# Performance work log

Hardware: AMD Instinct MI355X
Metric: run time of the kernel (lower is better)

The kernel has to match this reference:

```python
import jax, jax.numpy as jnp
import numpy as np
from functools import partial

GRAD_THR = 0.01
COUNT_THR = 3
MIN_PROB = 0.1
MAX_PROB = 0.9
FREE_PROB = 1e-10
HEIGHT_Q = 0.7


def prob2logodds(p):
    return jnp.log(p) - jnp.log1p(-p)


def shift_diff(x, d):
    # right neighbor minus left neighbor at dilation d (replicate padding on width)
    xp = jnp.pad(x, [(0, 0)] * (x.ndim - 1) + [(d, d)], mode='edge')
    return xp[..., 2 * d:] - xp[..., :-2 * d]


def assign_score(depth):
    rml_dx = jax.nn.relu(shift_diff(depth, 1))    # relu(right - left)
    lmr_dx = jax.nn.relu(-shift_diff(depth, 1))   # relu(left - right)
    rml_ddx = jax.nn.relu(-shift_diff(rml_dx, 2))  # relu(-(right-left))
    lmr_ddx = jax.nn.relu(shift_diff(lmr_dx, 2))   # relu(-(left-right))
    W = depth.shape[-1]
    grad_pos = jnp.concatenate([rml_ddx[..., :W // 2], lmr_ddx[..., W // 2:]], axis=-1)
    grad_neg = jnp.concatenate([lmr_ddx[..., :W // 2], rml_ddx[..., W // 2:]], axis=-1)
    return grad_pos, grad_neg


def _occupancy_one(xyz, score, g_mask, size, grad_thr, count_thr):
    # xyz: [3, N]; score, g_mask: [N]
    x, y, z = xyz[0], xyz[1], xyz[2]
    range_mask = (x >= 0) & (x <= size - 1) & (z >= 0) & (z <= size - 1)
    height_mask = y < jnp.quantile(y, HEIGHT_Q)
    valid = height_mask & range_mask
    obj = valid & (~g_mask) & (score > 0)
    ground = valid & g_mask
    xi = jnp.clip(x.astype(jnp.int32), 0, size - 1)
    zi = jnp.clip(z.astype(jnp.int32), 0, size - 1)
    idx = xi + size * zi  # [N] flat grid index
    G = size * size
    occ = jnp.zeros(G, jnp.float32).at[idx].add(
        jnp.where(obj & (score > grad_thr), 1.0, 0.0))
    norm = jnp.zeros(G, jnp.float32).at[idx].add(obj.astype(jnp.float32))
    gcnt = jnp.zeros(G, jnp.float32).at[idx].add(ground.astype(jnp.float32))
    free = (gcnt > 0) & (norm == 0)
    unknown = (~free) & (norm < count_thr)
    prob = occ / jnp.maximum(norm, 1.0)
    prob = jnp.where(unknown | free, 0.5, prob)
    return prob, free, unknown


def compute_occupancy_probability(scaled_ptcloud, ground_flat, disc_flat, size, grad_thr, count_thr):
    f = partial(_occupancy_one, size=size, grad_thr=grad_thr, count_thr=count_thr)
    return jax.vmap(f)(scaled_ptcloud, disc_flat, ground_flat)


def max_pool3x3(x):
    return jax.lax.reduce_window(
        x, -jnp.inf, jax.lax.max,
        (1, 1, 3, 3), (1, 1, 1, 1),
        [(0, 0), (0, 0), (1, 1), (1, 1)])


def setup_inputs() -> dict:
    key = jax.random.key(0)
    k1, k2, k3 = jax.random.split(key, 3)
    B, H, W, S = 32, 384, 1280, 256
    N = H * W
    depth = jax.random.uniform(k1, (B, 1, H, W), jnp.float32, 0.1, 80.0)
    ptc = jax.random.uniform(k2, (B, 3, N), jnp.float32, -5.0, float(S) + 5.0)
    gmask = jax.random.randint(k3, (B, 1, H, W), 0, 2).astype(bool)
    return {"depth": depth, "scaled_ptcloud": ptc, "ground_mask": gmask, "ogm_size": S}


def reference(depth, scaled_ptcloud, ground_mask, ogm_size):
    B = depth.shape[0]
    S = ogm_size
    prior_free_odds = prob2logodds(FREE_PROB)
    p_min_odds = prob2logodds(MIN_PROB)
    p_max_odds = prob2logodds(MAX_PROB)
    n_max_odds = prob2logodds(MAX_PROB)

    grad_pos, grad_neg = assign_score(depth)
    gp_flat = grad_pos.reshape(B, -1)
    gn_flat = grad_neg.reshape(B, -1)
    gm_flat = ground_mask.reshape(B, -1)

    pos_prob, free, unknown = compute_occupancy_probability(
        scaled_ptcloud, gm_flat, gp_flat, S, GRAD_THR, COUNT_THR)
    pos_odds = prob2logodds(pos_prob)
    pos_odds = jnp.where(free, prior_free_odds, pos_odds)
    pos_odds = jnp.where(unknown, 0.0, pos_odds)
    pos_odds = jnp.clip(pos_odds, p_min_odds, p_max_odds)

    neg_prob, _, _ = compute_occupancy_probability(
        scaled_ptcloud, gm_flat, gn_flat, S, GRAD_THR, COUNT_THR)
    neg_odds = prob2logodds(neg_prob)
    neg_odds = jnp.where(free | unknown, 0.0, neg_odds)
    neg_odds = jnp.clip(neg_odds, 0.0, n_max_odds)
    neg_odds = max_pool3x3(neg_odds.reshape(B, 1, S, S))

    return pos_odds.reshape(B, 1, S, S) - neg_odds
```

## Files before the change

kernel.cpp:

```cpp
#include <hip/hip_runtime.h>
#include <stdint.h>

#define H_    384
#define W_    1280
#define NPTS  (H_ * W_)
#define S_    256
#define G_    (S_ * S_)
#define NBH   32
#define NBC   32
#define NBS   480
#define NBF   64
#define NBINS 4096
#define QCAP  1024
#define LO_   (-16.0f)
#define INVW_ (4096.0f / 544.0f)
#define PMAX  2.1972246f
#define TX 64
#define TZ 16

typedef unsigned int u32;
typedef unsigned long long u64;
typedef unsigned char u8;
typedef float f32x4 __attribute__((ext_vector_type(4)));
typedef u32   u32x4 __attribute__((ext_vector_type(4)));

__device__ __forceinline__ u32 fkey(float f) {
    u32 u = __float_as_uint(f);
    return (u & 0x80000000u) ? ~u : (u | 0x80000000u);
}
__device__ __forceinline__ float keyfloat(u32 k) {
    u32 u = (k & 0x80000000u) ? (k ^ 0x80000000u) : ~k;
    return __uint_as_float(u);
}
__device__ __forceinline__ int lbin(float y) {
    int b = (int)floorf((y - LO_) * INVW_);
    return b < 0 ? 0 : (b > NBINS - 1 ? NBINS - 1 : b);
}
template<int NBB>
__device__ __forceinline__ void decode(int id, int& b, int& j) {
    const int r = id & 7;
    const int g8 = id >> 3;
    j = g8 % NBB;
    b = (g8 / NBB) * 8 + r;
}

__global__ void k_hist(const float* __restrict__ ptc, const u8* __restrict__ gmb,
                       u32* __restrict__ hgsum, u32* __restrict__ mode,
                       u32* __restrict__ pk, u8* __restrict__ gflag) {
    __shared__ u32 h[NBINS];
    int b, j; decode<NBH>((int)blockIdx.x, b, j);
    const int t = threadIdx.x;
    if (b == 0 && j == 0 && t < 64) {
        u32 v = ((const u32*)gmb)[t];
        bool bad = !(v == 0u || v == 1u || v == 0x3F800000u);
        u64 m = __ballot(bad);
        if (t == 0) *mode = (m == 0ULL) ? 1u : 0u;
    }
    {
        const u32x4 z4 = {0u, 0u, 0u, 0u};
        u32x4* pk4 = (u32x4*)(pk + (size_t)b * G_) + (size_t)j * (G_ / 4 / NBH);
        for (int k = t; k < G_ / 4 / NBH; k += 256) pk4[k] = z4;
        u32x4* gf4 = (u32x4*)(gflag + (size_t)b * G_) + (size_t)j * (G_ / 16 / NBH);
        if (t < G_ / 16 / NBH) gf4[t] = z4;
    }
    for (int k = t; k < NBINS; k += 256) h[k] = 0u;
    __syncthreads();
    const f32x4* y4 = (const f32x4*)(ptc + (size_t)b * 3 * NPTS + NPTS);
    for (int i = j * 256 + t; i < NPTS / 4; i += NBH * 256) {
        f32x4 v = y4[i];
        atomicAdd(&h[lbin(v.x)], 1u);
        atomicAdd(&h[lbin(v.y)], 1u);
        atomicAdd(&h[lbin(v.z)], 1u);
        atomicAdd(&h[lbin(v.w)], 1u);
    }
    __syncthreads();
    u32* dst = hgsum + (size_t)b * NBINS;
    for (int k = t; k < NBINS; k += 256)
        if (h[k]) atomicAdd(&dst[k], h[k]);
}

__global__ void k_find(const u32* __restrict__ hgsum, u32* __restrict__ fbuf, int ka) {
    __shared__ u32 h[NBINS];
    __shared__ u32 part[256];
    __shared__ u32 sres[4];
    const int t = threadIdx.x, b = blockIdx.x;
    const u32* src = hgsum + (size_t)b * NBINS;
    for (int k = t; k < NBINS; k += 256) h[k] = src[k];
    __syncthreads();
    u32 loc = 0;
#pragma unroll
    for (int q = 0; q < NBINS / 256; q++) loc += h[t * (NBINS / 256) + q];
    part[t] = loc;
    __syncthreads();
    for (int ofs = 1; ofs < 256; ofs <<= 1) {
        u32 v = (t >= ofs) ? part[t - ofs] : 0u;
        __syncthreads();
        part[t] += v;
        __syncthreads();
    }
    u32 before = part[t] - loc;
    const u32 ra = (u32)ka, rb = (u32)ka + 1u;
#pragma unroll
    for (int q = 0; q < NBINS / 256; q++) {
        const int jj = t * (NBINS / 256) + q;
        const u32 v = h[jj];
        if (before <= ra && ra < before + v) { sres[0] = (u32)jj; sres[1] = ra - before; }
        if (before <= rb && rb < before + v) { sres[2] = (u32)jj; sres[3] = rb - before; }
        before += v;
    }
    __syncthreads();
    if (t < 4) fbuf[b * 4 + t] = sres[t];
}

__global__ void k_collect(const float* __restrict__ ptc, const u32* __restrict__ fbuf,
                          u32* __restrict__ cnt, u32* __restrict__ cbuf) {
    int b, j; decode<NBC>((int)blockIdx.x, b, j);
    const int t = threadIdx.x;
    const int binA = (int)fbuf[b * 4 + 0];
    const int binB = (int)fbuf[b * 4 + 2];
    const bool twob = (binB != binA);
    const f32x4* y4 = (const f32x4*)(ptc + (size_t)b * 3 * NPTS + NPTS);
    u32* bufA = cbuf + (size_t)b * 2 * QCAP;
    u32* bufB = bufA + QCAP;
    for (int i = j * 256 + t; i < NPTS / 4; i += NBC * 256) {
        f32x4 v = y4[i];
        float f[4] = {v.x, v.y, v.z, v.w};
#pragma unroll
        for (int q = 0; q < 4; q++) {
            const int bn = lbin(f[q]);
            if (bn == binA) {
                u32 p = atomicAdd(&cnt[b * 2], 1u);
                if (p < QCAP) bufA[p] = fkey(f[q]);
            } else if (twob && bn == binB) {
                u32 p = atomicAdd(&cnt[b * 2 + 1], 1u);
                if (p < QCAP) bufB[p] = fkey(f[q]);
            }
        }
    }
}

__global__ void k_select(const u32* __restrict__ fbuf, const u32* __restrict__ cnt,
                         const u32* __restrict__ cbuf, float* __restrict__ tbuf,
                         float wlo, float whi) {
    __shared__ u32 sA[QCAP];
    __shared__ u32 sB[QCAP];
    __shared__ u32 skey[2];
    const int t = threadIdx.x, b = blockIdx.x;
    const u32 remA = fbuf[b * 4 + 1], remB = fbuf[b * 4 + 3];
    const bool twob = (fbuf[b * 4 + 0] != fbuf[b * 4 + 2]);
    u32 cA = cnt[b * 2];     if (cA > QCAP) cA = QCAP;
    u32 cB = cnt[b * 2 + 1]; if (cB > QCAP) cB = QCAP;
    const u32* bufA = cbuf + (size_t)b * 2 * QCAP;
    const u32* bufB = bufA + QCAP;
    for (u32 i = t; i < cA; i += 256) sA[i] = bufA[i];
    if (twob) for (u32 i = t; i < cB; i += 256) sB[i] = bufB[i];
    __syncthreads();
    for (u32 i = t; i < cA; i += 256) {
        const u32 k = sA[i];
        u32 less = 0, eq = 0;
        for (u32 jj = 0; jj < cA; jj++) { u32 kj = sA[jj]; less += (kj < k); eq += (kj == k); }
        if (less <= remA && remA < less + eq) skey[0] = k;
    }
    const u32* srcb = twob ? sB : sA;
    const u32 mB = twob ? cB : cA;
    for (u32 i = t; i < mB; i += 256) {
        const u32 k = srcb[i];
        u32 less = 0, eq = 0;
        for (u32 jj = 0; jj < mB; jj++) { u32 kj = srcb[jj]; less += (kj < k); eq += (kj == k); }
        if (less <= remB && remB < less + eq) skey[1] = k;
    }
    __syncthreads();
    if (t == 0) {
        float ylo = keyfloat(skey[0]);
        float yhi = keyfloat(skey[1]);
        tbuf[b] = __fadd_rn(__fmul_rn(ylo, wlo), __fmul_rn(yhi, whi));
    }
}

__global__ void k_scatter(const float* __restrict__ depth, const float* __restrict__ ptc,
                          const u8* __restrict__ gmb, const float* __restrict__ tbuf,
                          const u32* __restrict__ mode,
                          u32* __restrict__ pk, u8* __restrict__ gflag) {
    int b, j; decode<NBS>((int)blockIdx.x, b, j);
    const int t = threadIdx.x;
    const float st = tbuf[b];
    const u32 smode = *mode;
    const int i4 = j * 256 + t;
    const int i0 = i4 * 4;
    const size_t pb = (size_t)b * 3 * NPTS;

    const f32x4 yv = __builtin_nontemporal_load((const f32x4*)(ptc + pb + NPTS) + i4);
    const float fy[4] = {yv.x, yv.y, yv.z, yv.w};
    bool pass[4]; bool any = false;
#pragma unroll
    for (int q = 0; q < 4; q++) { pass[q] = fy[q] < st; any = any || pass[q]; }
    if (!any) return;

    const f32x4 xv = __builtin_nontemporal_load((const f32x4*)(ptc + pb) + i4);
    const f32x4 zv = __builtin_nontemporal_load((const f32x4*)(ptc + pb + 2 * NPTS) + i4);
    const float fx[4] = {xv.x, xv.y, xv.z, xv.w};
    const float fz[4] = {zv.x, zv.y, zv.z, zv.w};
    u32 gw[4];
    if (smode) {
        u32x4 gg = __builtin_nontemporal_load((const u32x4*)((const u32*)gmb + (size_t)b * NPTS) + i4);
        gw[0] = gg.x; gw[1] = gg.y; gw[2] = gg.z; gw[3] = gg.w;
    } else {
        u32 gg = __builtin_nontemporal_load((const u32*)(gmb + (size_t)b * NPTS) + i4);
        gw[0] = gg & 0xFFu; gw[1] = (gg >> 8) & 0xFFu; gw[2] = (gg >> 16) & 0xFFu; gw[3] = (gg >> 24) & 0xFFu;
    }

    const int colbase = i0 % W_;
    const float* drow = depth + (size_t)b * NPTS + (i0 - colbase);
    u32* pkb = pk + (size_t)b * G_;
    u8* gfb = gflag + (size_t)b * G_;

#pragma unroll
    for (int q = 0; q < 4; q++) {
        if (!pass[q]) continue;
        const float x = fx[q], z = fz[q];
        if (!(x >= 0.0f && x <= 255.0f && z >= 0.0f && z <= 255.0f)) continue;
        const int cell = (int)x + S_ * (int)z;
        if (gw[q]) { gfb[cell] = 1; continue; }

        const int col = colbase + q;
        int j1 = col - 2; if (j1 < 0) j1 = 0;
        int j2 = col + 2; if (j2 > W_ - 1) j2 = W_ - 1;
        int am = j1 - 1;  if (am < 0) am = 0;
        int ap = j1 + 1;  if (ap > W_ - 1) ap = W_ - 1;
        int bm = j2 - 1;  if (bm < 0) bm = 0;
        int bp = j2 + 1;  if (bp > W_ - 1) bp = W_ - 1;
        float a = drow[ap] - drow[am];
        float c = drow[bp] - drow[bm];
        float rml1 = fmaxf(a, 0.0f),  lmr1 = fmaxf(-a, 0.0f);
        float rml2 = fmaxf(c, 0.0f),  lmr2 = fmaxf(-c, 0.0f);
        float rddx = fmaxf(rml1 - rml2, 0.0f);
        float lddx = fmaxf(lmr2 - lmr1, 0.0f);
        float sp, sn;
        if (col < W_ / 2) { sp = rddx; sn = lddx; } else { sp = lddx; sn = rddx; }
        u32 p = (sp > 0.0f) ? (1u | ((u32)(sp > 0.01f) << 8)) : 0u;
        u32 n = (sn > 0.0f) ? ((1u << 16) | ((u32)(sn > 0.01f) << 24)) : 0u;
        const u32 inc = p | n;
        if (inc) atomicAdd(&pkb[cell], inc);
    }
}

__device__ __forceinline__ float neg_val(u32 w) {
    const u32 pn = w & 0xFFu;
    if (pn < 3u) return 0.0f;
    const u32 nn = (w >> 16) & 0xFFu;
    if (nn < 3u) return 0.0f;
    const u32 no = (w >> 24) & 0xFFu;
    float p = (float)no / (float)nn;
    float v = logf(p) - log1pf(-p);
    return fminf(fmaxf(v, 0.0f), PMAX);
}

__global__ void k_finalpool(const u32* __restrict__ pk, const u8* __restrict__ gflag,
                            float* __restrict__ out) {
    __shared__ float ng[(TZ + 2) * (TX + 2)];
    int b, j; decode<NBF>((int)blockIdx.x, b, j);
    const int t = threadIdx.x;
    const int x0 = (j & 3) * TX;
    const int z0 = (j >> 2) * TZ;
    const u32* pkb = pk + (size_t)b * G_;
    const u8* gfb = gflag + (size_t)b * G_;
    for (int idx = t; idx < (TZ + 2) * (TX + 2); idx += 256) {
        const int gx = x0 + idx % (TX + 2) - 1;
        const int gz = z0 + idx / (TX + 2) - 1;
        float v = -INFINITY;
        if (gx >= 0 && gx < S_ && gz >= 0 && gz < S_) v = neg_val(pkb[gx + S_ * gz]);
        ng[idx] = v;
    }
    __syncthreads();
    const int lx = t & 63;
    const int lz0 = (t >> 6) * 4;
#pragma unroll
    for (int k = 0; k < 4; k++) {
        const int lz = lz0 + k;
        const int cell = (x0 + lx) + S_ * (z0 + lz);
        const u32 w = pkb[cell];
        const u32 pn = w & 0xFFu;
        float po;
        if (pn < 3u) {
            po = (pn == 0u && gfb[cell]) ? -PMAX : 0.0f;
        } else {
            const u32 oc = (w >> 8) & 0xFFu;
            float p = (float)oc / (float)pn;
            float v = logf(p) - log1pf(-p);
            po = fminf(fmaxf(v, -PMAX), PMAX);
        }
        float mx = -INFINITY;
#pragma unroll
        for (int dz = 0; dz < 3; dz++)
#pragma unroll
            for (int dx = 0; dx < 3; dx++)
                mx = fmaxf(mx, ng[(lz + dz) * (TX + 2) + (lx + dx)]);
        out[(size_t)b * G_ + cell] = po - mx;
    }
}

extern "C" void kernel_launch(void* const* d_in, const int* in_sizes, int n_in,
                              void* d_out, int out_size, void* d_ws, size_t ws_size,
                              hipStream_t stream) {
    const float* depth = (const float*)d_in[0];
    const float* ptc   = (const float*)d_in[1];
    const u8* gm       = (const u8*)d_in[2];
    const int B = in_sizes[0] / NPTS;

    char* ws = (char*)d_ws;
    size_t off = 0;
    auto alloc = [&](size_t bytes) -> void* {
        void* p = ws + off; off += (bytes + 255) & ~(size_t)255; return p;
    };
    u32* hgsum = (u32*)alloc((size_t)B * NBINS * 4);
    u32* cnt   = (u32*)alloc((size_t)B * 2 * 4);
    const size_t zero_bytes = off;
    u32* pk    = (u32*)alloc((size_t)B * G_ * 4);
    u8*  gflag = (u8*)alloc((size_t)B * G_);
    u32* cbuf  = (u32*)alloc((size_t)B * 2 * QCAP * 4);
    float* tbuf= (float*)alloc((size_t)B * 4);
    u32* fbuf  = (u32*)alloc((size_t)B * 4 * 4);
    u32* mode  = (u32*)alloc(4);
    (void)ws_size; (void)n_in; (void)out_size;

    (void)hipMemsetAsync(d_ws, 0, zero_bytes, stream);

    const float idxf = 0.7f * (float)(NPTS - 1);
    const int   ka   = (int)floorf(idxf);
    const float whi  = idxf - (float)ka;
    const float wlo  = 1.0f - whi;

    k_hist    <<<dim3(NBH * B), dim3(256), 0, stream>>>(ptc, gm, hgsum, mode, pk, gflag);
    k_find    <<<dim3(B),       dim3(256), 0, stream>>>(hgsum, fbuf, ka);
    k_collect <<<dim3(NBC * B), dim3(256), 0, stream>>>(ptc, fbuf, cnt, cbuf);
    k_select  <<<dim3(B),       dim3(256), 0, stream>>>(fbuf, cnt, cbuf, tbuf, wlo, whi);
    k_scatter <<<dim3(NBS * B), dim3(256), 0, stream>>>(depth, ptc, gm, tbuf, mode, pk, gflag);
    k_finalpool<<<dim3(NBF * B), dim3(256), 0, stream>>>(pk, gflag, (float*)d_out);
}
```

Measured before the change: 512.5 us.

## Precompute per-pixel score and ground codes in histogram kernel for scatter

Moves the depth-gradient score and ground-mask evaluation out of the scatter kernel into the histogram kernel, which now reads depth with vector loads and writes a one-byte code per pixel. The scatter kernel then reads only one u32 per four points instead of scattered depth samples and the ground mask. The aim is to take the dependent gather loads off the scatter kernel's critical path and overlap that work with the histogram pass. In exchange the prep kernel always reads all of depth and the mask and writes an extra B*NPTS byte buffer, including for points that later fail the height test. Mode detection moves to a per-block shared flag.

Result: slower. 531.3 us (+3.7%).

```diff
diff --git a/kernel.cpp b/kernel.cpp
--- a/kernel.cpp
+++ b/kernel.cpp
@@ -7,6 +7,8 @@
 #define S_    256
 #define G_    (S_ * S_)
 #define NBH   32
+#define NSEG  (NPTS / NBH)
+#define NGRP  (NSEG / 4)
 #define NBC   32
 #define NBS   480
 #define NBF   64
@@ -44,18 +46,30 @@
     b = (g8 / NBB) * 8 + r;
 }
 
-__global__ void k_hist(const float* __restrict__ ptc, const u8* __restrict__ gmb,
-                       u32* __restrict__ hgsum, u32* __restrict__ mode,
-                       u32* __restrict__ pk, u8* __restrict__ gflag) {
+__device__ __forceinline__ u32 score_bits(float a, float cc, int col, u32 g) {
+    const float rml1 = fmaxf(a, 0.0f),  lmr1 = fmaxf(-a, 0.0f);
+    const float rml2 = fmaxf(cc, 0.0f), lmr2 = fmaxf(-cc, 0.0f);
+    const float rddx = fmaxf(rml1 - rml2, 0.0f);
+    const float lddx = fmaxf(lmr2 - lmr1, 0.0f);
+    float sp, sn;
+    if (col < W_ / 2) { sp = rddx; sn = lddx; } else { sp = lddx; sn = rddx; }
+    u32 c = 0;
+    c |= (sp > 0.0f)  ? 1u : 0u;
+    c |= (sp > 0.01f) ? 2u : 0u;
+    c |= (sn > 0.0f)  ? 4u : 0u;
+    c |= (sn > 0.01f) ? 8u : 0u;
+    c |= g ? 16u : 0u;
+    return c;
+}
+
+__global__ void k_prep(const float* __restrict__ depth, const float* __restrict__ ptc,
+                       const u8* __restrict__ gmb, u32* __restrict__ hgsum,
+                       u8* __restrict__ scode, u32* __restrict__ pk,
+                       u8* __restrict__ gflag) {
     __shared__ u32 h[NBINS];
+    __shared__ u32 smode;
     int b, j; decode<NBH>((int)blockIdx.x, b, j);
     const int t = threadIdx.x;
-    if (b == 0 && j == 0 && t < 64) {
-        u32 v = ((const u32*)gmb)[t];
-        bool bad = !(v == 0u || v == 1u || v == 0x3F800000u);
-        u64 m = __ballot(bad);
-        if (t == 0) *mode = (m == 0ULL) ? 1u : 0u;
-    }
     {
         const u32x4 z4 = {0u, 0u, 0u, 0u};
         u32x4* pk4 = (u32x4*)(pk + (size_t)b * G_) + (size_t)j * (G_ / 4 / NBH);
@@ -64,7 +78,65 @@
         if (t < G_ / 16 / NBH) gf4[t] = z4;
     }
     for (int k = t; k < NBINS; k += 256) h[k] = 0u;
-    __syncthreads();
+    if (t < 64) {
+        u32 v = ((const u32*)gmb)[t];
+        bool bad = !(v == 0u || v == 1u || v == 0x3F800000u);
+        u64 m = __ballot(bad);
+        if (t == 0) smode = (m == 0ULL) ? 1u : 0u;
+    }
+    __syncthreads();
+    const u32 md = smode;
+
+    const int seg0 = j * NSEG;
+    const float* dbat = depth + (size_t)b * NPTS;
+    const u32* gmw = (const u32*)gmb;
+    u32* sc4 = (u32*)(scode + (size_t)b * NPTS + seg0);
+    for (int gi = t; gi < NGRP; gi += 256) {
+        const int i0 = seg0 + gi * 4;
+        const int c0 = i0 % W_;
+        const float* dr = dbat + (i0 - c0);
+        float aa[4], cca[4];
+        if (c0 >= 4 && c0 <= W_ - 8) {
+            const f32x4 v0 = *(const f32x4*)(dr + c0 - 4);
+            const f32x4 v1 = *(const f32x4*)(dr + c0);
+            const f32x4 v2 = *(const f32x4*)(dr + c0 + 4);
+            const float w[12] = {v0.x, v0.y, v0.z, v0.w, v1.x, v1.y, v1.z, v1.w,
+                                 v2.x, v2.y, v2.z, v2.w};
+#pragma unroll
+            for (int q = 0; q < 4; q++) {
+                aa[q]  = w[q + 3] - w[q + 1];
+                cca[q] = w[q + 7] - w[q + 5];
+            }
+        } else {
+#pragma unroll
+            for (int q = 0; q < 4; q++) {
+                const int c = c0 + q;
+                int j1 = c - 2; if (j1 < 0) j1 = 0;
+                int j2 = c + 2; if (j2 > W_ - 1) j2 = W_ - 1;
+                int am = j1 - 1; if (am < 0) am = 0;
+                int ap = j1 + 1; if (ap > W_ - 1) ap = W_ - 1;
+                int bm = j2 - 1; if (bm < 0) bm = 0;
+                int bp = j2 + 1; if (bp > W_ - 1) bp = W_ - 1;
+                aa[q]  = dr[ap] - dr[am];
+                cca[q] = dr[bp] - dr[bm];
+            }
+        }
+        u32 gw[4];
+        if (md) {
+            const u32x4 gg = *(const u32x4*)(gmw + (size_t)b * NPTS + i0);
+            gw[0] = gg.x; gw[1] = gg.y; gw[2] = gg.z; gw[3] = gg.w;
+        } else {
+            const u32 gg = *(const u32*)(gmb + (size_t)b * NPTS + i0);
+            gw[0] = gg & 0xFFu; gw[1] = (gg >> 8) & 0xFFu;
+            gw[2] = (gg >> 16) & 0xFFu; gw[3] = (gg >> 24) & 0xFFu;
+        }
+        u32 code = 0;
+#pragma unroll
+        for (int q = 0; q < 4; q++)
+            code |= score_bits(aa[q], cca[q], c0 + q, gw[q]) << (8 * q);
+        __builtin_nontemporal_store(code, sc4 + gi);
+    }
+
     const f32x4* y4 = (const f32x4*)(ptc + (size_t)b * 3 * NPTS + NPTS);
     for (int i = j * 256 + t; i < NPTS / 4; i += NBH * 256) {
         f32x4 v = y4[i];
@@ -177,16 +249,13 @@
     }
 }
 
-__global__ void k_scatter(const float* __restrict__ depth, const float* __restrict__ ptc,
-                          const u8* __restrict__ gmb, const float* __restrict__ tbuf,
-                          const u32* __restrict__ mode,
+__global__ void k_scatter(const float* __restrict__ ptc, const float* __restrict__ tbuf,
+                          const u8* __restrict__ scode,
                           u32* __restrict__ pk, u8* __restrict__ gflag) {
     int b, j; decode<NBS>((int)blockIdx.x, b, j);
     const int t = threadIdx.x;
     const float st = tbuf[b];
-    const u32 smode = *mode;
     const int i4 = j * 256 + t;
-    const int i0 = i4 * 4;
     const size_t pb = (size_t)b * 3 * NPTS;
 
     const f32x4 yv = __builtin_nontemporal_load((const f32x4*)(ptc + pb + NPTS) + i4);
@@ -198,19 +267,10 @@
 
     const f32x4 xv = __builtin_nontemporal_load((const f32x4*)(ptc + pb) + i4);
     const f32x4 zv = __builtin_nontemporal_load((const f32x4*)(ptc + pb + 2 * NPTS) + i4);
+    const u32 code4 = __builtin_nontemporal_load((const u32*)(scode + (size_t)b * NPTS) + i4);
     const float fx[4] = {xv.x, xv.y, xv.z, xv.w};
     const float fz[4] = {zv.x, zv.y, zv.z, zv.w};
-    u32 gw[4];
-    if (smode) {
-        u32x4 gg = __builtin_nontemporal_load((const u32x4*)((const u32*)gmb + (size_t)b * NPTS) + i4);
-        gw[0] = gg.x; gw[1] = gg.y; gw[2] = gg.z; gw[3] = gg.w;
-    } else {
-        u32 gg = __builtin_nontemporal_load((const u32*)(gmb + (size_t)b * NPTS) + i4);
-        gw[0] = gg & 0xFFu; gw[1] = (gg >> 8) & 0xFFu; gw[2] = (gg >> 16) & 0xFFu; gw[3] = (gg >> 24) & 0xFFu;
-    }
-
-    const int colbase = i0 % W_;
-    const float* drow = depth + (size_t)b * NPTS + (i0 - colbase);
+
     u32* pkb = pk + (size_t)b * G_;
     u8* gfb = gflag + (size_t)b * G_;
 
@@ -220,25 +280,10 @@
         const float x = fx[q], z = fz[q];
         if (!(x >= 0.0f && x <= 255.0f && z >= 0.0f && z <= 255.0f)) continue;
         const int cell = (int)x + S_ * (int)z;
-        if (gw[q]) { gfb[cell] = 1; continue; }
-
-        const int col = colbase + q;
-        int j1 = col - 2; if (j1 < 0) j1 = 0;
-        int j2 = col + 2; if (j2 > W_ - 1) j2 = W_ - 1;
-        int am = j1 - 1;  if (am < 0) am = 0;
-        int ap = j1 + 1;  if (ap > W_ - 1) ap = W_ - 1;
-        int bm = j2 - 1;  if (bm < 0) bm = 0;
-        int bp = j2 + 1;  if (bp > W_ - 1) bp = W_ - 1;
-        float a = drow[ap] - drow[am];
-        float c = drow[bp] - drow[bm];
-        float rml1 = fmaxf(a, 0.0f),  lmr1 = fmaxf(-a, 0.0f);
-        float rml2 = fmaxf(c, 0.0f),  lmr2 = fmaxf(-c, 0.0f);
-        float rddx = fmaxf(rml1 - rml2, 0.0f);
-        float lddx = fmaxf(lmr2 - lmr1, 0.0f);
-        float sp, sn;
-        if (col < W_ / 2) { sp = rddx; sn = lddx; } else { sp = lddx; sn = rddx; }
-        u32 p = (sp > 0.0f) ? (1u | ((u32)(sp > 0.01f) << 8)) : 0u;
-        u32 n = (sn > 0.0f) ? ((1u << 16) | ((u32)(sn > 0.01f) << 24)) : 0u;
+        const u32 cq = (code4 >> (8 * q)) & 0xFFu;
+        if (cq & 16u) { gfb[cell] = 1; continue; }
+        u32 p = (cq & 1u) ? (1u | (((cq >> 1) & 1u) << 8)) : 0u;
+        u32 n = (cq & 4u) ? ((1u << 16) | (((cq >> 3) & 1u) << 24)) : 0u;
         const u32 inc = p | n;
         if (inc) atomicAdd(&pkb[cell], inc);
     }
@@ -320,7 +365,7 @@
     u32* cbuf  = (u32*)alloc((size_t)B * 2 * QCAP * 4);
     float* tbuf= (float*)alloc((size_t)B * 4);
     u32* fbuf  = (u32*)alloc((size_t)B * 4 * 4);
-    u32* mode  = (u32*)alloc(4);
+    u8* scode  = (u8*)alloc((size_t)B * NPTS);
     (void)ws_size; (void)n_in; (void)out_size;
 
     (void)hipMemsetAsync(d_ws, 0, zero_bytes, stream);
@@ -330,10 +375,10 @@
     const float whi  = idxf - (float)ka;
     const float wlo  = 1.0f - whi;
 
-    k_hist    <<<dim3(NBH * B), dim3(256), 0, stream>>>(ptc, gm, hgsum, mode, pk, gflag);
+    k_prep    <<<dim3(NBH * B), dim3(256), 0, stream>>>(depth, ptc, gm, hgsum, scode, pk, gflag);
     k_find    <<<dim3(B),       dim3(256), 0, stream>>>(hgsum, fbuf, ka);
     k_collect <<<dim3(NBC * B), dim3(256), 0, stream>>>(ptc, fbuf, cnt, cbuf);
     k_select  <<<dim3(B),       dim3(256), 0, stream>>>(fbuf, cnt, cbuf, tbuf, wlo, whi);
-    k_scatter <<<dim3(NBS * B), dim3(256), 0, stream>>>(depth, ptc, gm, tbuf, mode, pk, gflag);
+    k_scatter <<<dim3(NBS * B), dim3(256), 0, stream>>>(ptc, tbuf, scode, pk, gflag);
     k_finalpool<<<dim3(NBF * B), dim3(256), 0, stream>>>(pk, gflag, (float*)d_out);
 }
```

## Fuse bin-find and select into collect kernel, pack ground flag into counts

Applied to the files above, without the earlier changes.

Each collect block now recomputes the quantile bin search from the global histogram with a wave-shuffle scan. The last block per batch, detected through an atomic done counter, performs the exact selection, which removes the separate find and select launches. The ground flag byte array is replaced by the top bit of the packed count word, set with atomicOr, so the flag zeroing and the extra reads in the final kernel go away. The costs are a redundant bin search in every collect block, a last-block-done pattern that depends on correct memory fences, and atomics on the ground path.

New measurement: 690.7 us. 1.35x slower.

```diff
diff --git a/kernel.cpp b/kernel.cpp
--- a/kernel.cpp
+++ b/kernel.cpp
@@ -24,6 +24,7 @@
 typedef float f32x4 __attribute__((ext_vector_type(4)));
 typedef u32   u32x4 __attribute__((ext_vector_type(4)));
 
+
 __device__ __forceinline__ u32 fkey(float f) {
     u32 u = __float_as_uint(f);
     return (u & 0x80000000u) ? ~u : (u | 0x80000000u);
@@ -44,9 +45,9 @@
     b = (g8 / NBB) * 8 + r;
 }
 
-__global__ void k_hist(const float* __restrict__ ptc, const u8* __restrict__ gmb,
+__global__ void k_prep(const float* __restrict__ ptc, const u8* __restrict__ gmb,
                        u32* __restrict__ hgsum, u32* __restrict__ mode,
-                       u32* __restrict__ pk, u8* __restrict__ gflag) {
+                       u32* __restrict__ pk) {
     __shared__ u32 h[NBINS];
     int b, j; decode<NBH>((int)blockIdx.x, b, j);
     const int t = threadIdx.x;
@@ -60,8 +61,6 @@
         const u32x4 z4 = {0u, 0u, 0u, 0u};
         u32x4* pk4 = (u32x4*)(pk + (size_t)b * G_) + (size_t)j * (G_ / 4 / NBH);
         for (int k = t; k < G_ / 4 / NBH; k += 256) pk4[k] = z4;
-        u32x4* gf4 = (u32x4*)(gflag + (size_t)b * G_) + (size_t)j * (G_ / 16 / NBH);
-        if (t < G_ / 16 / NBH) gf4[t] = z4;
     }
     for (int k = t; k < NBINS; k += 256) h[k] = 0u;
     __syncthreads();
@@ -79,46 +78,54 @@
         if (h[k]) atomicAdd(&dst[k], h[k]);
 }
 
-__global__ void k_find(const u32* __restrict__ hgsum, u32* __restrict__ fbuf, int ka) {
-    __shared__ u32 h[NBINS];
-    __shared__ u32 part[256];
+__device__ __forceinline__ void find_bins(const u32* __restrict__ hgsum, int b, int ka,
+                                          u32* sres, u32* swsum) {
+    const int t = threadIdx.x, lane = t & 63, w = t >> 6;
+    const u32x4* src = (const u32x4*)(hgsum + (size_t)b * NBINS) + t * 4;
+    const u32x4 a0 = src[0], a1 = src[1], a2 = src[2], a3 = src[3];
+    u32 v[16] = {a0.x, a0.y, a0.z, a0.w, a1.x, a1.y, a1.z, a1.w,
+                 a2.x, a2.y, a2.z, a2.w, a3.x, a3.y, a3.z, a3.w};
+    u32 loc = 0;
+#pragma unroll
+    for (int q = 0; q < 16; q++) loc += v[q];
+    u32 inc = loc;
+#pragma unroll
+    for (int off = 1; off < 64; off <<= 1) {
+        u32 n = __shfl_up(inc, off);
+        if (lane >= off) inc += n;
+    }
+    if (lane == 63) swsum[w] = inc;
+    __syncthreads();
+    u32 before = inc - loc;
+    for (int k = 0; k < w; k++) before += swsum[k];
+    const u32 ra = (u32)ka, rb = (u32)ka + 1u;
+#pragma unroll
+    for (int q = 0; q < 16; q++) {
+        const u32 c = v[q];
+        if (before <= ra && ra < before + c) { sres[0] = (u32)(t * 16 + q); sres[1] = ra - before; }
+        if (before <= rb && rb < before + c) { sres[2] = (u32)(t * 16 + q); sres[3] = rb - before; }
+        before += c;
+    }
+    __syncthreads();
+}
+
+__global__ void k_collect(const float* __restrict__ ptc, const u32* __restrict__ hgsum,
+                          u32* __restrict__ cnt, u32* __restrict__ cbuf,
+                          u32* __restrict__ done, float* __restrict__ tbuf,
+                          int ka, float wlo, float whi) {
     __shared__ u32 sres[4];
-    const int t = threadIdx.x, b = blockIdx.x;
-    const u32* src = hgsum + (size_t)b * NBINS;
-    for (int k = t; k < NBINS; k += 256) h[k] = src[k];
-    __syncthreads();
-    u32 loc = 0;
-#pragma unroll
-    for (int q = 0; q < NBINS / 256; q++) loc += h[t * (NBINS / 256) + q];
-    part[t] = loc;
-    __syncthreads();
-    for (int ofs = 1; ofs < 256; ofs <<= 1) {
-        u32 v = (t >= ofs) ? part[t - ofs] : 0u;
-        __syncthreads();
-        part[t] += v;
-        __syncthreads();
-    }
-    u32 before = part[t] - loc;
-    const u32 ra = (u32)ka, rb = (u32)ka + 1u;
-#pragma unroll
-    for (int q = 0; q < NBINS / 256; q++) {
-        const int jj = t * (NBINS / 256) + q;
-        const u32 v = h[jj];
-        if (before <= ra && ra < before + v) { sres[0] = (u32)jj; sres[1] = ra - before; }
-        if (before <= rb && rb < before + v) { sres[2] = (u32)jj; sres[3] = rb - before; }
-        before += v;
-    }
-    __syncthreads();
-    if (t < 4) fbuf[b * 4 + t] = sres[t];
-}
-
-__global__ void k_collect(const float* __restrict__ ptc, const u32* __restrict__ fbuf,
-                          u32* __restrict__ cnt, u32* __restrict__ cbuf) {
+    __shared__ u32 swsum[4];
+    __shared__ u32 sAB[2 * QCAP];
+    __shared__ u32 skey[2];
+    __shared__ u32 scc[2];
+    __shared__ int lastflag;
     int b, j; decode<NBC>((int)blockIdx.x, b, j);
     const int t = threadIdx.x;
-    const int binA = (int)fbuf[b * 4 + 0];
-    const int binB = (int)fbuf[b * 4 + 2];
+
+    find_bins(hgsum, b, ka, sres, swsum);
+    const int binA = (int)sres[0], binB = (int)sres[2];
     const bool twob = (binB != binA);
+
     const f32x4* y4 = (const f32x4*)(ptc + (size_t)b * 3 * NPTS + NPTS);
     u32* bufA = cbuf + (size_t)b * 2 * QCAP;
     u32* bufB = bufA + QCAP;
@@ -130,28 +137,33 @@
             const int bn = lbin(f[q]);
             if (bn == binA) {
                 u32 p = atomicAdd(&cnt[b * 2], 1u);
-                if (p < QCAP) bufA[p] = fkey(f[q]);
+                if (p < QCAP) atomicExch(&bufA[p], fkey(f[q]));
             } else if (twob && bn == binB) {
                 u32 p = atomicAdd(&cnt[b * 2 + 1], 1u);
-                if (p < QCAP) bufB[p] = fkey(f[q]);
+                if (p < QCAP) atomicExch(&bufB[p], fkey(f[q]));
             }
         }
     }
-}
-
-__global__ void k_select(const u32* __restrict__ fbuf, const u32* __restrict__ cnt,
-                         const u32* __restrict__ cbuf, float* __restrict__ tbuf,
-                         float wlo, float whi) {
-    __shared__ u32 sA[QCAP];
-    __shared__ u32 sB[QCAP];
-    __shared__ u32 skey[2];
-    const int t = threadIdx.x, b = blockIdx.x;
-    const u32 remA = fbuf[b * 4 + 1], remB = fbuf[b * 4 + 3];
-    const bool twob = (fbuf[b * 4 + 0] != fbuf[b * 4 + 2]);
-    u32 cA = cnt[b * 2];     if (cA > QCAP) cA = QCAP;
-    u32 cB = cnt[b * 2 + 1]; if (cB > QCAP) cB = QCAP;
-    const u32* bufA = cbuf + (size_t)b * 2 * QCAP;
-    const u32* bufB = bufA + QCAP;
+
+    __syncthreads();
+    if (t == 0) {
+        __threadfence();
+        u32 old = atomicAdd(&done[b], 1u);
+        lastflag = (old == (u32)(NBC - 1)) ? 1 : 0;
+        if (lastflag) {
+            __threadfence();
+            scc[0] = atomicAdd(&cnt[b * 2], 0u);
+            scc[1] = atomicAdd(&cnt[b * 2 + 1], 0u);
+        }
+    }
+    __syncthreads();
+    if (!lastflag) return;
+
+    const u32 remA = sres[1], remB = sres[3];
+    u32 cA = scc[0]; if (cA > QCAP) cA = QCAP;
+    u32 cB = scc[1]; if (cB > QCAP) cB = QCAP;
+    u32* sA = sAB;
+    u32* sB = sAB + QCAP;
     for (u32 i = t; i < cA; i += 256) sA[i] = bufA[i];
     if (twob) for (u32 i = t; i < cB; i += 256) sB[i] = bufB[i];
     __syncthreads();
@@ -179,8 +191,7 @@
 
 __global__ void k_scatter(const float* __restrict__ depth, const float* __restrict__ ptc,
                           const u8* __restrict__ gmb, const float* __restrict__ tbuf,
-                          const u32* __restrict__ mode,
-                          u32* __restrict__ pk, u8* __restrict__ gflag) {
+                          const u32* __restrict__ mode, u32* __restrict__ pk) {
     int b, j; decode<NBS>((int)blockIdx.x, b, j);
     const int t = threadIdx.x;
     const float st = tbuf[b];
@@ -212,7 +223,6 @@
     const int colbase = i0 % W_;
     const float* drow = depth + (size_t)b * NPTS + (i0 - colbase);
     u32* pkb = pk + (size_t)b * G_;
-    u8* gfb = gflag + (size_t)b * G_;
 
 #pragma unroll
     for (int q = 0; q < 4; q++) {
@@ -220,7 +230,7 @@
         const float x = fx[q], z = fz[q];
         if (!(x >= 0.0f && x <= 255.0f && z >= 0.0f && z <= 255.0f)) continue;
         const int cell = (int)x + S_ * (int)z;
-        if (gw[q]) { gfb[cell] = 1; continue; }
+        if (gw[q]) { atomicOr(&pkb[cell], 0x80000000u); continue; }
 
         const int col = colbase + q;
         int j1 = col - 2; if (j1 < 0) j1 = 0;
@@ -249,21 +259,19 @@
     if (pn < 3u) return 0.0f;
     const u32 nn = (w >> 16) & 0xFFu;
     if (nn < 3u) return 0.0f;
-    const u32 no = (w >> 24) & 0xFFu;
+    const u32 no = (w >> 24) & 0x7Fu;
     float p = (float)no / (float)nn;
     float v = logf(p) - log1pf(-p);
     return fminf(fmaxf(v, 0.0f), PMAX);
 }
 
-__global__ void k_finalpool(const u32* __restrict__ pk, const u8* __restrict__ gflag,
-                            float* __restrict__ out) {
+__global__ void k_finalpool(const u32* __restrict__ pk, float* __restrict__ out) {
     __shared__ float ng[(TZ + 2) * (TX + 2)];
     int b, j; decode<NBF>((int)blockIdx.x, b, j);
     const int t = threadIdx.x;
     const int x0 = (j & 3) * TX;
     const int z0 = (j >> 2) * TZ;
     const u32* pkb = pk + (size_t)b * G_;
-    const u8* gfb = gflag + (size_t)b * G_;
     for (int idx = t; idx < (TZ + 2) * (TX + 2); idx += 256) {
         const int gx = x0 + idx % (TX + 2) - 1;
         const int gz = z0 + idx / (TX + 2) - 1;
@@ -282,7 +290,7 @@
         const u32 pn = w & 0xFFu;
         float po;
         if (pn < 3u) {
-            po = (pn == 0u && gfb[cell]) ? -PMAX : 0.0f;
+            po = (pn == 0u && (w >> 31)) ? -PMAX : 0.0f;
         } else {
             const u32 oc = (w >> 8) & 0xFFu;
             float p = (float)oc / (float)pn;
@@ -314,12 +322,11 @@
     };
     u32* hgsum = (u32*)alloc((size_t)B * NBINS * 4);
     u32* cnt   = (u32*)alloc((size_t)B * 2 * 4);
+    u32* done  = (u32*)alloc((size_t)B * 4);
     const size_t zero_bytes = off;
     u32* pk    = (u32*)alloc((size_t)B * G_ * 4);
-    u8*  gflag = (u8*)alloc((size_t)B * G_);
     u32* cbuf  = (u32*)alloc((size_t)B * 2 * QCAP * 4);
     float* tbuf= (float*)alloc((size_t)B * 4);
-    u32* fbuf  = (u32*)alloc((size_t)B * 4 * 4);
     u32* mode  = (u32*)alloc(4);
     (void)ws_size; (void)n_in; (void)out_size;
 
@@ -330,10 +337,9 @@
     const float whi  = idxf - (float)ka;
     const float wlo  = 1.0f - whi;
 
-    k_hist    <<<dim3(NBH * B), dim3(256), 0, stream>>>(ptc, gm, hgsum, mode, pk, gflag);
-    k_find    <<<dim3(B),       dim3(256), 0, stream>>>(hgsum, fbuf, ka);
-    k_collect <<<dim3(NBC * B), dim3(256), 0, stream>>>(ptc, fbuf, cnt, cbuf);
-    k_select  <<<dim3(B),       dim3(256), 0, stream>>>(fbuf, cnt, cbuf, tbuf, wlo, whi);
-    k_scatter <<<dim3(NBS * B), dim3(256), 0, stream>>>(depth, ptc, gm, tbuf, mode, pk, gflag);
-    k_finalpool<<<dim3(NBF * B), dim3(256), 0, stream>>>(pk, gflag, (float*)d_out);
-}
+    k_prep    <<<dim3(NBH * B), dim3(256), 0, stream>>>(ptc, gm, hgsum, mode, pk);
+    k_collect <<<dim3(NBC * B), dim3(256), 0, stream>>>(ptc, hgsum, cnt, cbuf, done, tbuf,
+                                                        ka, wlo, whi);
+    k_scatter <<<dim3(NBS * B), dim3(256), 0, stream>>>(depth, ptc, gm, tbuf, mode, pk);
+    k_finalpool<<<dim3(NBF * B), dim3(256), 0, stream>>>(pk, (float*)d_out);
+}
```
